# Kernel tuning notes

Measured on AMD Instinct MI355X. Metric: run time of the kernel, lower is better.

The kernel has to match this reference:

```python
import jax, jax.numpy as jnp
import numpy as np

TWO_PI = 2.0 * np.pi


def _unwrap(x):
    # torch: abs(x - 2*pi*round(x/(2*pi))) -> wrap to principal value, take magnitude
    return jnp.abs(x - TWO_PI * jnp.round(x / TWO_PI))


def _shift_diff_last(x):
    # Equivalent to matmul with M = triu(1,d=1)-triu(1,d=2)-eye (superdiag=+1, diag=-1):
    # out[..., 0] = -x[..., 0]; out[..., j] = x[..., j-1] - x[..., j]
    return jnp.concatenate([-x[..., :1], x[..., :-1] - x[..., 1:]], axis=-1)


def setup_inputs() -> dict:
    key = jax.random.key(0)
    k1, k2, k3, k4 = jax.random.split(key, 4)
    shape = (32, 1, 513, 512)  # [B, 1, nfreqs, frames]
    return {
        "spec_est_real": jax.random.normal(k1, shape, dtype=jnp.float32),
        "spec_est_imag": jax.random.normal(k2, shape, dtype=jnp.float32),
        "spec_ref_real": jax.random.normal(k3, shape, dtype=jnp.float32),
        "spec_ref_imag": jax.random.normal(k4, shape, dtype=jnp.float32),
    }


def reference(spec_est_real, spec_est_imag, spec_ref_real, spec_ref_imag):
    # torch.angle(complex).squeeze(1) -> [B, F, T]
    phase_g = jnp.arctan2(spec_est_imag, spec_est_real)[:, 0]
    phase_r = jnp.arctan2(spec_ref_imag, spec_ref_real)[:, 0]

    d = phase_r - phase_g  # [B, F, T]

    # IP loss
    ip_loss = jnp.mean(_unwrap(d))
    # GD: shift-difference along freq axis (GD_r - GD_g = shift_diff(phase_r - phase_g))
    gd_loss = jnp.mean(_unwrap(_shift_diff_last(jnp.swapaxes(d, 1, 2))))
    # PTD: shift-difference along time axis
    ptd_loss = jnp.mean(_unwrap(_shift_diff_last(d)))

    return ip_loss + gd_loss + ptd_loss
```

## Files before the change

### kernel.cpp

```cpp
#include <hip/hip_runtime.h>
#include <math.h>


#define NB 32
#define NF 513
#define NT 512
#define RPW 4
#define CHUNKS 129
#define NBLOCKS 1032
#define NTOT 8404992LL

static __device__ __forceinline__ float fast_atan2(float y, float x) {
    const float PI_F  = 3.14159274101257324f;
    const float PI_2F = 1.57079632679489662f;
    float ax = fabsf(x), ay = fabsf(y);
    float mx = fmaxf(ax, ay), mn = fminf(ax, ay);
    float r  = mn * __builtin_amdgcn_rcpf(mx);
    r = (mx == 0.f) ? 0.f : r;
    float s = r * r;
    float p = fmaf(s, -0.01172120f, 0.05265332f);
    p = fmaf(s, p, -0.11643287f);
    p = fmaf(s, p,  0.19354346f);
    p = fmaf(s, p, -0.33262347f);
    p = fmaf(s, p,  0.99997726f);
    float a = r * p;
    a = (ay > ax) ? (PI_2F - a) : a;
    a = (x < 0.f) ? (PI_F - a) : a;
    return copysignf(a, y);
}

static __device__ __forceinline__ float pdiff(float a, float b, float c, float d) {
    return fast_atan2(fmaf(d, a, -(c * b)), fmaf(c, a, d * b));
}

static __device__ __forceinline__ float wrap_abs(float x) {
    const float PI_F     = 3.14159274101257324f;
    const float TWO_PI_F = 6.28318548202514648f;
    float u = fabsf(x);
    return u > PI_F ? TWO_PI_F - u : u;
}

struct Row8 { float4 a0, a1, b0, b1, c0, c1, e0, e1; };

static __device__ __forceinline__ void calc8(const Row8& r, float d[8]) {
    d[0] = pdiff(r.a0.x, r.b0.x, r.c0.x, r.e0.x);
    d[1] = pdiff(r.a0.y, r.b0.y, r.c0.y, r.e0.y);
    d[2] = pdiff(r.a0.z, r.b0.z, r.c0.z, r.e0.z);
    d[3] = pdiff(r.a0.w, r.b0.w, r.c0.w, r.e0.w);
    d[4] = pdiff(r.a1.x, r.b1.x, r.c1.x, r.e1.x);
    d[5] = pdiff(r.a1.y, r.b1.y, r.c1.y, r.e1.y);
    d[6] = pdiff(r.a1.z, r.b1.z, r.c1.z, r.e1.z);
    d[7] = pdiff(r.a1.w, r.b1.w, r.c1.w, r.e1.w);
}

__global__ __launch_bounds__(256) void phase_loss_k(
    const float* __restrict__ er, const float* __restrict__ ei,
    const float* __restrict__ rr, const float* __restrict__ ri,
    float* __restrict__ slots)
{
    const int tid  = threadIdx.x;
    const int lane = tid & 63;
    const int wid  = (blockIdx.x << 2) | (tid >> 6);
    const int b    = wid / CHUNKS;
    const int f0   = (wid - b * CHUNKS) * RPW;
    const int base = b * (NF * NT);

#define LOAD_ROW(dst, f_) do {                                   \
        const int _i = base + (f_) * NT + lane * 8;              \
        dst.a0 = *(const float4*)(er + _i);                      \
        dst.a1 = *(const float4*)(er + _i + 4);                  \
        dst.b0 = *(const float4*)(ei + _i);                      \
        dst.b1 = *(const float4*)(ei + _i + 4);                  \
        dst.c0 = *(const float4*)(rr + _i);                      \
        dst.c1 = *(const float4*)(rr + _i + 4);                  \
        dst.e0 = *(const float4*)(ri + _i);                      \
        dst.e1 = *(const float4*)(ri + _i + 4);                  \
    } while (0)

    float s = 0.f;
    float dp[8];
    Row8 cur, nxt;

    if (f0 > 0) LOAD_ROW(cur, f0 - 1);
    LOAD_ROW(nxt, f0);
    if (f0 > 0) {
        calc8(cur, dp);
    } else {
        #pragma unroll
        for (int k = 0; k < 8; ++k) dp[k] = 0.f;
    }

    #pragma unroll
    for (int r = 0; r < RPW; ++r) {
        const int f = f0 + r;
        if (f >= NF) break;
        cur = nxt;
        if (r + 1 < RPW && f + 1 < NF) LOAD_ROW(nxt, f + 1);
        float d[8];
        calc8(cur, d);
        float dt = __shfl_up(d[7], 1, 64);
        if (lane == 0) dt = 0.f;
        #pragma unroll
        for (int k = 0; k < 8; ++k) {
            s += fabsf(d[k]);
            s += wrap_abs(dp[k] - d[k]);
            s += wrap_abs(dt - d[k]);
            dt = d[k];
            dp[k] = d[k];
        }
    }
#undef LOAD_ROW

    #pragma unroll
    for (int off = 32; off > 0; off >>= 1)
        s += __shfl_down(s, off, 64);
    __shared__ float ws4[4];
    if (lane == 0) ws4[tid >> 6] = s;
    __syncthreads();
    if (tid == 0) slots[blockIdx.x] = ws4[0] + ws4[1] + ws4[2] + ws4[3];
}

__global__ __launch_bounds__(256) void finalize_k(const float* __restrict__ slots,
                                                  float* __restrict__ out)
{
    int tid = threadIdx.x;
    float s = 0.f;
    for (int i = tid; i < NBLOCKS; i += 256) s += slots[i];
    #pragma unroll
    for (int off = 32; off > 0; off >>= 1)
        s += __shfl_down(s, off, 64);
    __shared__ float wsum[4];
    if ((tid & 63) == 0) wsum[tid >> 6] = s;
    __syncthreads();
    if (tid == 0) {
        double tot = (double)wsum[0] + (double)wsum[1] + (double)wsum[2] + (double)wsum[3];
        out[0] = (float)(tot / (double)NTOT);
    }
}

extern "C" void kernel_launch(void* const* d_in, const int* in_sizes, int n_in,
                              void* d_out, int out_size, void* d_ws, size_t ws_size,
                              hipStream_t stream) {
    const float* er = (const float*)d_in[0];
    const float* ei = (const float*)d_in[1];
    const float* rr = (const float*)d_in[2];
    const float* ri = (const float*)d_in[3];
    float* out   = (float*)d_out;
    float* slots = (float*)d_ws;

    phase_loss_k<<<NBLOCKS, 256, 0, stream>>>(er, ei, rr, ri, slots);
    finalize_k<<<1, 256, 0, stream>>>(slots, out);
}
```

Measured before the change: 35.15 us.

## Process two row-chunks per wave with interleaved loads and compute

Each wave now handles two independent 4-row frequency chunks. Row loads for one chunk are interleaved with the atan2 and accumulation work of the other, so memory latency is hidden within the wave. The block count is halved and launch bounds request 2 blocks per CU. This gives more memory-level parallelism per wave but raises register pressure and cuts the total wave count, which may lower occupancy.

```diff
diff --git a/kernel.cpp b/kernel.cpp
--- a/kernel.cpp
+++ b/kernel.cpp
@@ -7,7 +7,9 @@
 #define NT 512
 #define RPW 4
 #define CHUNKS 129
-#define NBLOCKS 1032
+#define NSTREAMS 4128
+#define NWAVES 2064
+#define NBLOCKS 516
 #define NTOT 8404992LL
 
 static __device__ __forceinline__ float fast_atan2(float y, float x) {
@@ -53,7 +55,22 @@
     d[7] = pdiff(r.a1.w, r.b1.w, r.c1.w, r.e1.w);
 }
 
-__global__ __launch_bounds__(256) void phase_loss_k(
+static __device__ __forceinline__ float acc_row(const float d[8], float dp[8], int lane) {
+    float dt = __shfl_up(d[7], 1, 64);
+    if (lane == 0) dt = 0.f;
+    float s = 0.f;
+    #pragma unroll
+    for (int k = 0; k < 8; ++k) {
+        s += fabsf(d[k]);
+        s += wrap_abs(dp[k] - d[k]);
+        s += wrap_abs(dt - d[k]);
+        dt = d[k];
+        dp[k] = d[k];
+    }
+    return s;
+}
+
+__global__ __launch_bounds__(256, 2) void phase_loss_k(
     const float* __restrict__ er, const float* __restrict__ ei,
     const float* __restrict__ rr, const float* __restrict__ ri,
     float* __restrict__ slots)
@@ -61,12 +78,15 @@
     const int tid  = threadIdx.x;
     const int lane = tid & 63;
     const int wid  = (blockIdx.x << 2) | (tid >> 6);
-    const int b    = wid / CHUNKS;
-    const int f0   = (wid - b * CHUNKS) * RPW;
-    const int base = b * (NF * NT);
+    const int sa = wid * 2, sb = sa + 1;
+    const int ba = sa / CHUNKS,            bb = sb / CHUNKS;
+    const int f0a = (sa - ba * CHUNKS) * RPW, f0b = (sb - bb * CHUNKS) * RPW;
+    const int basea = ba * (NF * NT),      baseb = bb * (NF * NT);
+    const int nva = (NF - f0a < RPW) ? (NF - f0a) : RPW;
+    const int nvb = (NF - f0b < RPW) ? (NF - f0b) : RPW;
 
-#define LOAD_ROW(dst, f_) do {                                   \
-        const int _i = base + (f_) * NT + lane * 8;              \
+#define LOAD_ROW(dst, base_, f_) do {                            \
+        const int _i = (base_) + (f_) * NT + lane * 8;           \
         dst.a0 = *(const float4*)(er + _i);                      \
         dst.a1 = *(const float4*)(er + _i + 4);                  \
         dst.b0 = *(const float4*)(ei + _i);                      \
@@ -78,37 +98,40 @@
     } while (0)
 
     float s = 0.f;
-    float dp[8];
-    Row8 cur, nxt;
+    float dpa[8], dpb[8], da[8], db[8];
+    Row8 Ra, Rb;
 
-    if (f0 > 0) LOAD_ROW(cur, f0 - 1);
-    LOAD_ROW(nxt, f0);
-    if (f0 > 0) {
-        calc8(cur, dp);
+    if (f0a > 0) LOAD_ROW(Ra, basea, f0a - 1);
+    if (f0b > 0) LOAD_ROW(Rb, baseb, f0b - 1);
+    if (f0a > 0) {
+        calc8(Ra, dpa);
     } else {
         #pragma unroll
-        for (int k = 0; k < 8; ++k) dp[k] = 0.f;
+        for (int k = 0; k < 8; ++k) dpa[k] = 0.f;
     }
+    LOAD_ROW(Ra, basea, f0a);
+    if (f0b > 0) {
+        calc8(Rb, dpb);
+    } else {
+        #pragma unroll
+        for (int k = 0; k < 8; ++k) dpb[k] = 0.f;
+    }
+    LOAD_ROW(Rb, baseb, f0b);
 
-    #pragma unroll
-    for (int r = 0; r < RPW; ++r) {
-        const int f = f0 + r;
-        if (f >= NF) break;
-        cur = nxt;
-        if (r + 1 < RPW && f + 1 < NF) LOAD_ROW(nxt, f + 1);
-        float d[8];
-        calc8(cur, d);
-        float dt = __shfl_up(d[7], 1, 64);
-        if (lane == 0) dt = 0.f;
-        #pragma unroll
-        for (int k = 0; k < 8; ++k) {
-            s += fabsf(d[k]);
-            s += wrap_abs(dp[k] - d[k]);
-            s += wrap_abs(dt - d[k]);
-            dt = d[k];
-            dp[k] = d[k];
-        }
-    }
+    calc8(Ra, da);  s += acc_row(da, dpa, lane);
+    if (nva > 1) LOAD_ROW(Ra, basea, f0a + 1);
+    calc8(Rb, db);  s += acc_row(db, dpb, lane);
+    if (nvb > 1) LOAD_ROW(Rb, baseb, f0b + 1);
+    if (nva > 1) { calc8(Ra, da);  s += acc_row(da, dpa, lane); }
+    if (nva > 2) LOAD_ROW(Ra, basea, f0a + 2);
+    if (nvb > 1) { calc8(Rb, db);  s += acc_row(db, dpb, lane); }
+    if (nvb > 2) LOAD_ROW(Rb, baseb, f0b + 2);
+    if (nva > 2) { calc8(Ra, da);  s += acc_row(da, dpa, lane); }
+    if (nva > 3) LOAD_ROW(Ra, basea, f0a + 3);
+    if (nvb > 2) { calc8(Rb, db);  s += acc_row(db, dpb, lane); }
+    if (nvb > 3) LOAD_ROW(Rb, baseb, f0b + 3);
+    if (nva > 3) { calc8(Ra, da);  s += acc_row(da, dpa, lane); }
+    if (nvb > 3) { calc8(Rb, db);  s += acc_row(db, dpb, lane); }
 #undef LOAD_ROW
 
     #pragma unroll
```

After: 35.85 us. Within noise of the previous version (+2.0%).

## Share halo rows between waves via LDS to cut redundant loads

Applied to the files above, without the earlier changes.

Each block now covers a 32-row frequency chunk, with each wave handling 8 consecutive rows. Each wave computes its last row first and publishes the phase difference to shared memory, so the next wave can use it as its previous row instead of reloading and recomputing it. Only the first wave of each block loads an extra halo row, which cuts redundant global reads and atan2 work from 1 in 4 rows to about 1 in 32. In exchange the kernel has half as many blocks, adds a block-wide barrier before the main loop, and carries a longer per-wave dependency chain with less latency hiding.

```diff
diff --git a/kernel.cpp b/kernel.cpp
--- a/kernel.cpp
+++ b/kernel.cpp
@@ -5,9 +5,9 @@
 #define NB 32
 #define NF 513
 #define NT 512
-#define RPW 4
-#define CHUNKS 129
-#define NBLOCKS 1032
+#define BPC 32
+#define CHUNKS 17
+#define NBLOCKS 544
 #define NTOT 8404992LL
 
 static __device__ __forceinline__ float fast_atan2(float y, float x) {
@@ -53,17 +53,38 @@
     d[7] = pdiff(r.a1.w, r.b1.w, r.c1.w, r.e1.w);
 }
 
+static __device__ __forceinline__ float acc_row(const float d[8], float dp[8], int lane) {
+    float dt = __shfl_up(d[7], 1, 64);
+    if (lane == 0) dt = 0.f;
+    float s = 0.f;
+    #pragma unroll
+    for (int k = 0; k < 8; ++k) {
+        s += fabsf(d[k]);
+        s += wrap_abs(dp[k] - d[k]);
+        s += wrap_abs(dt - d[k]);
+        dt = d[k];
+        dp[k] = d[k];
+    }
+    return s;
+}
+
 __global__ __launch_bounds__(256) void phase_loss_k(
     const float* __restrict__ er, const float* __restrict__ ei,
     const float* __restrict__ rr, const float* __restrict__ ri,
     float* __restrict__ slots)
 {
+    __shared__ float halo[4][NT];
+    __shared__ float ws4[4];
     const int tid  = threadIdx.x;
     const int lane = tid & 63;
-    const int wid  = (blockIdx.x << 2) | (tid >> 6);
+    const int wave = tid >> 6;
+    const int wid  = blockIdx.x;
     const int b    = wid / CHUNKS;
-    const int f0   = (wid - b * CHUNKS) * RPW;
+    const int f0b  = (wid - b * CHUNKS) * BPC;
+    const int f0w  = f0b + wave * 8;
     const int base = b * (NF * NT);
+    const int rem  = NF - f0w;
+    const int nv   = rem < 8 ? (rem < 0 ? 0 : rem) : 8;
 
 #define LOAD_ROW(dst, f_) do {                                   \
         const int _i = base + (f_) * NT + lane * 8;              \
@@ -77,45 +98,61 @@
         dst.e1 = *(const float4*)(ri + _i + 4);                  \
     } while (0)
 
+    Row8 R7, Rh;
+    const bool full  = (nv == 8);
+    const bool whalo = (wave == 0) && (f0b > 0) && (nv > 0);
+    if (full)  LOAD_ROW(R7, f0w + 7);
+    if (whalo) LOAD_ROW(Rh, f0b - 1);
+
+    float d7[8];
+    if (full) {
+        calc8(R7, d7);
+        if (wave < 3) {
+            *(float4*)&halo[wave + 1][lane * 8]     = make_float4(d7[0], d7[1], d7[2], d7[3]);
+            *(float4*)&halo[wave + 1][lane * 8 + 4] = make_float4(d7[4], d7[5], d7[6], d7[7]);
+        }
+    }
+    if (whalo) {
+        float dh[8];
+        calc8(Rh, dh);
+        *(float4*)&halo[0][lane * 8]     = make_float4(dh[0], dh[1], dh[2], dh[3]);
+        *(float4*)&halo[0][lane * 8 + 4] = make_float4(dh[4], dh[5], dh[6], dh[7]);
+    }
+    __syncthreads();
+
     float s = 0.f;
-    float dp[8];
-    Row8 cur, nxt;
+    if (nv > 0) {
+        float dp[8];
+        if (f0w > 0) {
+            float4 h0 = *(const float4*)&halo[wave][lane * 8];
+            float4 h1 = *(const float4*)&halo[wave][lane * 8 + 4];
+            dp[0] = h0.x; dp[1] = h0.y; dp[2] = h0.z; dp[3] = h0.w;
+            dp[4] = h1.x; dp[5] = h1.y; dp[6] = h1.z; dp[7] = h1.w;
+        } else {
+            #pragma unroll
+            for (int k = 0; k < 8; ++k) dp[k] = 0.f;
+        }
 
-    if (f0 > 0) LOAD_ROW(cur, f0 - 1);
-    LOAD_ROW(nxt, f0);
-    if (f0 > 0) {
-        calc8(cur, dp);
-    } else {
+        const int nfresh = full ? 7 : nv;
+        Row8 cur, nxt;
+        LOAD_ROW(nxt, f0w);
         #pragma unroll
-        for (int k = 0; k < 8; ++k) dp[k] = 0.f;
-    }
-
-    #pragma unroll
-    for (int r = 0; r < RPW; ++r) {
-        const int f = f0 + r;
-        if (f >= NF) break;
-        cur = nxt;
-        if (r + 1 < RPW && f + 1 < NF) LOAD_ROW(nxt, f + 1);
-        float d[8];
-        calc8(cur, d);
-        float dt = __shfl_up(d[7], 1, 64);
-        if (lane == 0) dt = 0.f;
-        #pragma unroll
-        for (int k = 0; k < 8; ++k) {
-            s += fabsf(d[k]);
-            s += wrap_abs(dp[k] - d[k]);
-            s += wrap_abs(dt - d[k]);
-            dt = d[k];
-            dp[k] = d[k];
+        for (int r = 0; r < 7; ++r) {
+            if (r >= nfresh) break;
+            cur = nxt;
+            if (r + 1 < nfresh) LOAD_ROW(nxt, f0w + r + 1);
+            float d[8];
+            calc8(cur, d);
+            s += acc_row(d, dp, lane);
         }
+        if (full) s += acc_row(d7, dp, lane);
     }
 #undef LOAD_ROW
 
     #pragma unroll
     for (int off = 32; off > 0; off >>= 1)
         s += __shfl_down(s, off, 64);
-    __shared__ float ws4[4];
-    if (lane == 0) ws4[tid >> 6] = s;
+    if (lane == 0) ws4[wave] = s;
     __syncthreads();
     if (tid == 0) slots[blockIdx.x] = ws4[0] + ws4[1] + ws4[2] + ws4[3];
 }
```

New measurement: 33.89 us. 1.04x faster.
